# Kernel tuning notes

Hardware: AMD Instinct MI355X
Metric: run time of the kernel (lower is better)

Reference implementation:

```python
import jax, jax.numpy as jnp
import numpy as np

B = 1048576
C = 15


def setup_inputs() -> dict:
    key = jax.random.key(0)
    k1, k2 = jax.random.split(key)
    output = jax.random.normal(k1, (B, C), dtype=jnp.float32)
    labels = jax.random.randint(k2, (B, C), 0, 2, dtype=jnp.int64)
    return {"output": output, "labels": labels}


def reference(output, labels):
    # output: [B, C] logits; labels: [B, C] binary multi-label {0,1}
    dt = output.dtype
    outs = jax.nn.sigmoid(output)  # original uses output[:, :C] == full output here

    pos = (labels == 1).astype(dt)  # [B, C]
    neg = (labels == 0).astype(dt)
    n_pos = pos.sum(axis=0)          # [C]
    n_neg = neg.sum(axis=0)
    mean_pos = (outs * pos).sum(axis=0) / jnp.maximum(n_pos, 1.0)
    mean_neg = (outs * neg).sum(axis=0) / jnp.maximum(n_neg, 1.0)

    # torch loop: mean over pos x neg of (1 - (pos - neg)) == 1 - mean(pos) + mean(neg)
    # edge cases: no pos -> 1 + mean(neg); no neg -> 1 - mean(pos)
    penalty = jnp.where(n_pos == 0, 1.0 + mean_neg,
                        jnp.where(n_neg == 0, 1.0 - mean_pos,
                                  1.0 - mean_pos + mean_neg))  # [C]
    sum_term = penalty.sum()

    # SoftMaxLoss: NLLLoss(log_softmax(output), argmax(labels, axis=1))
    labels1 = jnp.argmax(labels, axis=1)  # [B]
    logp = jax.nn.log_softmax(output, axis=1)
    ce = -jnp.take_along_axis(logp, labels1[:, None], axis=1).mean()

    cls = ce + 0.1 * (sum_term / 15.0)
    return (cls, 0.1 * penalty[-1])
```

## Files before the change

kernel.cpp:

```cpp
#include <hip/hip_runtime.h>

#define BLOCK 128
#define TILE  128
#define NC    15
#define TILE_FLOATS (TILE * NC)
#define TILE_BYTES  (TILE_FLOATS * 4)
#define CHUNKS      (TILE_BYTES / 16)
#define NACC  46
#define GRID  1024
#define NBLK  GRID

__device__ __forceinline__ void gld16(const void* g, void* l) {
    auto gp = (const __attribute__((address_space(1))) unsigned int*)g;
    auto lp = (__attribute__((address_space(3))) unsigned int*)l;
    __builtin_amdgcn_global_load_lds(gp, lp, 16, 0, 0);
}

__global__ __launch_bounds__(BLOCK) void auch_main(
    const float* __restrict__ logits,
    const int* __restrict__ labels,
    float* __restrict__ ws,
    int tpb)
{
    __shared__ __align__(16) float s_log[2][TILE_FLOATS];
    __shared__ __align__(16) int   s_lab[2][TILE_FLOATS];
    __shared__ float s_red[2][NACC];

    const int tid = threadIdx.x;
    const int tile0 = blockIdx.x * tpb;

    float acc[NACC];
#pragma unroll
    for (int i = 0; i < NACC; ++i) acc[i] = 0.f;

    {
        const char* gl = (const char*)logits + (size_t)tile0 * TILE_BYTES;
        const char* gb = (const char*)labels + (size_t)tile0 * TILE_BYTES;
        for (int i = tid; i < CHUNKS; i += BLOCK) {
            gld16(gl + i * 16, (char*)&s_log[0][0] + i * 16);
            gld16(gb + i * 16, (char*)&s_lab[0][0] + i * 16);
        }
    }

    int cur = 0;
    for (int t = 0; t < tpb; ++t) {
        if (t + 1 < tpb) {
            const char* gl = (const char*)logits + (size_t)(tile0 + t + 1) * TILE_BYTES;
            const char* gb = (const char*)labels + (size_t)(tile0 + t + 1) * TILE_BYTES;
            for (int i = tid; i < CHUNKS; i += BLOCK) {
                gld16(gl + i * 16, (char*)&s_log[cur ^ 1][0] + i * 16);
                gld16(gb + i * 16, (char*)&s_lab[cur ^ 1][0] + i * 16);
            }
            asm volatile("s_waitcnt vmcnt(8)" ::: "memory");
        } else {
            asm volatile("s_waitcnt vmcnt(0)" ::: "memory");
        }
        __builtin_amdgcn_sched_barrier(0);
        __builtin_amdgcn_s_barrier();
        __builtin_amdgcn_sched_barrier(0);

        const float* xr = &s_log[cur][tid * NC];
        const int*   lr = &s_lab[cur][tid * NC];
        float x[NC]; int lb[NC];
#pragma unroll
        for (int c = 0; c < NC; ++c) { x[c] = xr[c]; lb[c] = lr[c]; }

        float se = 0.f;
#pragma unroll
        for (int c = 0; c < NC; ++c) {
            float e = __expf(x[c]);
            se += e;
            float s = e * __builtin_amdgcn_rcpf(1.f + e);
            acc[c]      += lb[c] ? s : 0.f;
            acc[15 + c] += s;
            acc[30 + c] += lb[c] ? 1.f : 0.f;
        }
        float xsel = x[0];
#pragma unroll
        for (int c = NC - 1; c >= 1; --c) xsel = lb[c] ? x[c] : xsel;
        acc[45] += __logf(se) - xsel;

        __builtin_amdgcn_s_barrier();
        __builtin_amdgcn_sched_barrier(0);
        cur ^= 1;
    }

#pragma unroll
    for (int v = 0; v < NACC; ++v) {
#pragma unroll
        for (int off = 32; off > 0; off >>= 1)
            acc[v] += __shfl_xor(acc[v], off);
    }
    const int wave = tid >> 6, lane = tid & 63;
    if (lane == 0) {
#pragma unroll
        for (int v = 0; v < NACC; ++v) s_red[wave][v] = acc[v];
    }
    __syncthreads();
    if (tid < NACC)
        ws[tid * NBLK + blockIdx.x] = s_red[0][tid] + s_red[1][tid];
}

__global__ void auch_finalize(const float* __restrict__ ws, float* __restrict__ out, float Bf)
{
    __shared__ float s_val[NACC];
    const int tid = threadIdx.x;
    const int wave = tid >> 6, lane = tid & 63;
    for (int v = wave; v < NACC; v += 4) {
        float s = 0.f;
#pragma unroll
        for (int k = 0; k < NBLK / 64; ++k)
            s += ws[v * NBLK + lane + 64 * k];
#pragma unroll
        for (int off = 32; off > 0; off >>= 1) s += __shfl_xor(s, off);
        if (lane == 0) s_val[v] = s;
    }
    __syncthreads();
    if (tid == 0) {
        float sum_term = 0.f, pen14 = 0.f;
#pragma unroll
        for (int c = 0; c < NC; ++c) {
            float sp = s_val[c];
            float sa = s_val[15 + c];
            float np = s_val[30 + c];
            float sn = sa - sp;
            float nn = Bf - np;
            float mp = sp / fmaxf(np, 1.f);
            float mn = sn / fmaxf(nn, 1.f);
            float pen = (np == 0.f) ? (1.f + mn)
                       : ((nn == 0.f) ? (1.f - mp) : (1.f - mp + mn));
            sum_term += pen;
            if (c == NC - 1) pen14 = pen;
        }
        float ce = s_val[45] / Bf;
        out[0] = ce + 0.1f * (sum_term / 15.f);
        out[1] = 0.1f * pen14;
    }
}

extern "C" void kernel_launch(void* const* d_in, const int* in_sizes, int n_in,
                              void* d_out, int out_size, void* d_ws, size_t ws_size,
                              hipStream_t stream)
{
    const float* logits = (const float*)d_in[0];
    const int*   labels = (const int*)d_in[1];
    float* ws  = (float*)d_ws;
    float* out = (float*)d_out;

    const long long total = in_sizes[0];
    const int brows  = (int)(total / NC);
    const int ntiles = brows / TILE;
    const int tpb    = ntiles / GRID;

    hipMemsetAsync(d_ws, 0, NACC * NBLK * sizeof(float), stream);

    auch_main<<<GRID, BLOCK, 0, stream>>>(logits, labels, ws, tpb);
    auch_finalize<<<1, 256, 0, stream>>>(ws, out, (float)brows);
}
```

Before: 45.55 us.

## Restructure main kernel to per-wave pipelines with register-loaded packed labels

```diff
diff --git a/kernel.cpp b/kernel.cpp
--- a/kernel.cpp
+++ b/kernel.cpp
@@ -1,14 +1,15 @@
 #include <hip/hip_runtime.h>
 
-#define BLOCK 128
-#define TILE  128
-#define NC    15
-#define TILE_FLOATS (TILE * NC)
-#define TILE_BYTES  (TILE_FLOATS * 4)
-#define CHUNKS      (TILE_BYTES / 16)
-#define NACC  46
+#define BLOCK 256
+#define WPB   4
 #define GRID  1024
 #define NBLK  GRID
+#define NC    15
+#define TPW   4
+#define WREG  9600
+#define NACC  46
+
+typedef int int4v __attribute__((ext_vector_type(4)));
 
 __device__ __forceinline__ void gld16(const void* g, void* l) {
     auto gp = (const __attribute__((address_space(1))) unsigned int*)g;
@@ -16,54 +17,98 @@
     __builtin_amdgcn_global_load_lds(gp, lp, 16, 0, 0);
 }
 
-__global__ __launch_bounds__(BLOCK) void auch_main(
+__global__ __launch_bounds__(BLOCK, 4) void auch_main(
     const float* __restrict__ logits,
     const int* __restrict__ labels,
-    float* __restrict__ ws,
-    int tpb)
+    float* __restrict__ ws)
 {
-    __shared__ __align__(16) float s_log[2][TILE_FLOATS];
-    __shared__ __align__(16) int   s_lab[2][TILE_FLOATS];
-    __shared__ float s_red[2][NACC];
-
-    const int tid = threadIdx.x;
-    const int tile0 = blockIdx.x * tpb;
-
-    float acc[NACC];
-#pragma unroll
-    for (int i = 0; i < NACC; ++i) acc[i] = 0.f;
+    __shared__ __align__(16) char smem[WPB * WREG + 16];
+    __shared__ float s_red[WPB][NACC];
+
+    const int tid  = threadIdx.x;
+    const int wave = tid >> 6;
+    const int lane = tid & 63;
+    const int gw   = blockIdx.x * WPB + wave;
+
+    char* wbase = smem + wave * WREG;
+    const size_t wrow0 = (size_t)gw * (TPW * 64);
+
+    float accp[NC], acca[NC], accce = 0.f;
+    int npos[NC];
+#pragma unroll
+    for (int c = 0; c < NC; ++c) { accp[c] = 0.f; acca[c] = 0.f; npos[c] = 0; }
+
+    int4v L[2][4];
 
     {
-        const char* gl = (const char*)logits + (size_t)tile0 * TILE_BYTES;
-        const char* gb = (const char*)labels + (size_t)tile0 * TILE_BYTES;
-        for (int i = tid; i < CHUNKS; i += BLOCK) {
-            gld16(gl + i * 16, (char*)&s_log[0][0] + i * 16);
-            gld16(gb + i * 16, (char*)&s_lab[0][0] + i * 16);
-        }
-    }
-
-    int cur = 0;
-    for (int t = 0; t < tpb; ++t) {
-        if (t + 1 < tpb) {
-            const char* gl = (const char*)logits + (size_t)(tile0 + t + 1) * TILE_BYTES;
-            const char* gb = (const char*)labels + (size_t)(tile0 + t + 1) * TILE_BYTES;
-            for (int i = tid; i < CHUNKS; i += BLOCK) {
-                gld16(gl + i * 16, (char*)&s_log[cur ^ 1][0] + i * 16);
-                gld16(gb + i * 16, (char*)&s_lab[cur ^ 1][0] + i * 16);
+        const size_t eb = wrow0 * NC;
+#pragma unroll
+        for (int k = 0; k < 4; ++k) {
+            if (k < 3 || lane < 48) {
+                gld16(logits + eb + k * 256 + 4 * lane, wbase + k * 1024);
+                asm volatile("global_load_dwordx4 %0, %1, off"
+                             : "=v"(L[0][k])
+                             : "v"(labels + eb + k * 256 + 4 * lane));
+            }
+        }
+    }
+
+#pragma unroll
+    for (int t = 0; t < TPW; ++t) {
+        const int buf = t & 1;
+
+        if (t + 1 < TPW) {
+            const int nb = (t + 1) & 1;
+            const size_t eb = (wrow0 + (size_t)(t + 1) * 64) * NC;
+#pragma unroll
+            for (int k = 0; k < 4; ++k) {
+                if (k < 3 || lane < 48) {
+                    gld16(logits + eb + k * 256 + 4 * lane,
+                          wbase + (nb ? 4800 : 0) + k * 1024);
+                    asm volatile("global_load_dwordx4 %0, %1, off"
+                                 : "=v"(L[nb][k])
+                                 : "v"(labels + eb + k * 256 + 4 * lane));
+                }
             }
             asm volatile("s_waitcnt vmcnt(8)" ::: "memory");
         } else {
             asm volatile("s_waitcnt vmcnt(0)" ::: "memory");
         }
         __builtin_amdgcn_sched_barrier(0);
-        __builtin_amdgcn_s_barrier();
-        __builtin_amdgcn_sched_barrier(0);
-
-        const float* xr = &s_log[cur][tid * NC];
-        const int*   lr = &s_lab[cur][tid * NC];
-        float x[NC]; int lb[NC];
-#pragma unroll
-        for (int c = 0; c < NC; ++c) { x[c] = xr[c]; lb[c] = lr[c]; }
+
+        {
+            unsigned* lw = (unsigned*)(wbase + (buf ? 8640 : 3840));
+#pragma unroll
+            for (int k = 0; k < 4; ++k) {
+                if (k < 3 || lane < 48) {
+                    int4v v = L[buf][k];
+                    lw[k * 64 + lane] = (unsigned)(v.x & 1)
+                                      | ((unsigned)(v.y & 1) << 8)
+                                      | ((unsigned)(v.z & 1) << 16)
+                                      | ((unsigned)(v.w & 1) << 24);
+                }
+            }
+        }
+
+        const float* xr = (const float*)(wbase + (buf ? 4800 : 0)) + lane * NC;
+        float x[NC];
+#pragma unroll
+        for (int c = 0; c < NC; ++c) x[c] = xr[c];
+
+        const unsigned* lwr = (const unsigned*)(wbase + (buf ? 8640 : 3840));
+        const int bb = lane * NC;
+        unsigned w5[5];
+#pragma unroll
+        for (int j = 0; j < 5; ++j) w5[j] = lwr[(bb >> 2) + j];
+        const unsigned sh = (unsigned)(bb & 3) * 8u;
+        unsigned rb[4];
+#pragma unroll
+        for (int k = 0; k < 4; ++k)
+            rb[k] = (unsigned)((((unsigned long long)w5[k + 1] << 32) | w5[k]) >> sh);
+
+        int lb[NC];
+#pragma unroll
+        for (int c = 0; c < NC; ++c) lb[c] = (rb[c >> 2] >> ((c & 3) * 8)) & 1;
 
         float se = 0.f;
 #pragma unroll
@@ -71,34 +116,38 @@
             float e = __expf(x[c]);
             se += e;
             float s = e * __builtin_amdgcn_rcpf(1.f + e);
-            acc[c]      += lb[c] ? s : 0.f;
-            acc[15 + c] += s;
-            acc[30 + c] += lb[c] ? 1.f : 0.f;
+            accp[c] += lb[c] ? s : 0.f;
+            acca[c] += s;
+            npos[c] += (int)__popcll(__ballot(lb[c]));
         }
         float xsel = x[0];
 #pragma unroll
         for (int c = NC - 1; c >= 1; --c) xsel = lb[c] ? x[c] : xsel;
-        acc[45] += __logf(se) - xsel;
-
-        __builtin_amdgcn_s_barrier();
-        __builtin_amdgcn_sched_barrier(0);
-        cur ^= 1;
-    }
-
-#pragma unroll
-    for (int v = 0; v < NACC; ++v) {
-#pragma unroll
-        for (int off = 32; off > 0; off >>= 1)
-            acc[v] += __shfl_xor(acc[v], off);
-    }
-    const int wave = tid >> 6, lane = tid & 63;
+        accce += __logf(se) - xsel;
+    }
+
+#pragma unroll
+    for (int off = 32; off > 0; off >>= 1) {
+#pragma unroll
+        for (int c = 0; c < NC; ++c) {
+            accp[c] += __shfl_xor(accp[c], off);
+            acca[c] += __shfl_xor(acca[c], off);
+        }
+        accce += __shfl_xor(accce, off);
+    }
     if (lane == 0) {
 #pragma unroll
-        for (int v = 0; v < NACC; ++v) s_red[wave][v] = acc[v];
+        for (int c = 0; c < NC; ++c) {
+            s_red[wave][c]      = accp[c];
+            s_red[wave][15 + c] = acca[c];
+            s_red[wave][30 + c] = (float)npos[c];
+        }
+        s_red[wave][45] = accce;
     }
     __syncthreads();
     if (tid < NACC)
-        ws[tid * NBLK + blockIdx.x] = s_red[0][tid] + s_red[1][tid];
+        ws[tid * NBLK + blockIdx.x] = s_red[0][tid] + s_red[1][tid]
+                                    + s_red[2][tid] + s_red[3][tid];
 }
 
 __global__ void auch_finalize(const float* __restrict__ ws, float* __restrict__ out, float Bf)
@@ -148,12 +197,8 @@
     float* out = (float*)d_out;
 
     const long long total = in_sizes[0];
-    const int brows  = (int)(total / NC);
-    const int ntiles = brows / TILE;
-    const int tpb    = ntiles / GRID;
-
-    hipMemsetAsync(d_ws, 0, NACC * NBLK * sizeof(float), stream);
-
-    auch_main<<<GRID, BLOCK, 0, stream>>>(logits, labels, ws, tpb);
+    const int brows = (int)(total / NC);
+
+    auch_main<<<GRID, BLOCK, 0, stream>>>(logits, labels, ws);
     auch_finalize<<<1, 256, 0, stream>>>(ws, out, (float)brows);
 }
```

After: 43.43 us. 1.05x faster.
